# Performance work log

Hardware: AMD Instinct MI355X
Metric: run time of the kernel (lower is better)

Reference implementation:

```python
import jax, jax.numpy as jnp
import numpy as np

B, S, DIN, DOUT = 8, 2048, 512, 512

def setup_inputs() -> dict:
    key = jax.random.key(0)
    ks = jax.random.split(key, 9)
    s = 1.0 / np.sqrt(DIN)  # torch Linear default init scale
    return {
        "Q": jax.random.normal(ks[0], (B, S, DIN), jnp.float32),
        "K": jax.random.normal(ks[1], (B, S, DIN), jnp.float32),
        "V": jax.random.normal(ks[2], (B, S, DIN), jnp.float32),
        "Wq": jax.random.uniform(ks[3], (DIN, DOUT), jnp.float32, -s, s),
        "bq": jax.random.uniform(ks[4], (DOUT,), jnp.float32, -s, s),
        "Wk": jax.random.uniform(ks[5], (DIN, DOUT), jnp.float32, -s, s),
        "bk": jax.random.uniform(ks[6], (DOUT,), jnp.float32, -s, s),
        "Wv": jax.random.uniform(ks[7], (DIN, DOUT), jnp.float32, -s, s),
        "bv": jax.random.uniform(ks[8], (DOUT,), jnp.float32, -s, s),
    }

def reference(Q, K, V, Wq, bq, Wk, bk, Wv, bv):
    q = Q @ Wq + bq  # [B,S,D]
    k = K @ Wk + bk
    v = V @ Wv + bv
    # Unscaled attention, exactly as in the torch module
    attn = jnp.einsum('bqd,bkd->bqk', q, k)  # [B,S,S]
    attn_prob = jax.nn.softmax(attn, axis=-1)
    return jnp.einsum('bqk,bkd->bqd', attn_prob, v)
```

## Files before the change

kernel.cpp:

```cpp
#include <hip/hip_runtime.h>
#include <hip/hip_bf16.h>
#include <hip/hip_fp16.h>

#define B_ 8
#define S_ 2048
#define D_ 512

typedef _Float16 f16x8 __attribute__((ext_vector_type(8)));
typedef float f32x4 __attribute__((ext_vector_type(4)));

__device__ __forceinline__ void gload16(const void* g, void* l) {
    __builtin_amdgcn_global_load_lds(
        (const __attribute__((address_space(1))) void*)g,
        (__attribute__((address_space(3))) void*)l, 16, 0, 0);
}

__global__ void wconv_kernel(const float* __restrict__ Wq,
                             const float* __restrict__ Wk,
                             const float* __restrict__ Wv,
                             _Float16* __restrict__ w_ws) {
    int idx = blockIdx.x * 256 + threadIdx.x;
    int which = blockIdx.y;
    const float* W = (which == 0) ? Wq : (which == 1) ? Wk : Wv;
    int n = idx >> 9;
    int k = idx & 511;
    w_ws[(size_t)which * D_ * D_ + (size_t)n * D_ + k] = (_Float16)W[(size_t)k * D_ + n];
}

__launch_bounds__(256)
__global__ void proj_kernel(const float* __restrict__ Q,
                            const float* __restrict__ K,
                            const float* __restrict__ V,
                            const _Float16* __restrict__ w_ws,
                            const float* __restrict__ bq,
                            const float* __restrict__ bk,
                            const float* __restrict__ bv,
                            _Float16* __restrict__ q_ws,
                            _Float16* __restrict__ k_ws,
                            _Float16* __restrict__ v_ws) {
    __shared__ __align__(16) float    As[128 * 32];
    __shared__ __align__(16) _Float16 Bs[128 * 32];

    const int which = blockIdx.z;
    const float* X    = (which == 0) ? Q  : (which == 1) ? K  : V;
    const float* bias = (which == 0) ? bq : (which == 1) ? bk : bv;
    const _Float16* Wt = w_ws + (size_t)which * D_ * D_;

    const int Nb = blockIdx.x * 128;
    const int Mb = blockIdx.y * 128;
    const int t = threadIdx.x;
    const int w = t >> 6;
    const int l = t & 63;
    const int lr = l & 15;
    const int lk = (l >> 4) * 8;
    const int lq = (l >> 4) * 4;

    f32x4 acc[2][8] = {};

    for (int k0 = 0; k0 < D_; k0 += 32) {
        {
            int c = t;
#pragma unroll
            for (int i = 0; i < 4; i++, c += 256) {
                int row = c >> 3, p = c & 7;
                gload16(X + (size_t)(Mb + row) * D_ + k0 + ((p ^ (row & 7)) << 2),
                        As + c * 4);
            }
        }
        {
            int c = t;
#pragma unroll
            for (int i = 0; i < 2; i++, c += 256) {
                int col = c >> 2, p = c & 3;
                gload16(Wt + (size_t)(Nb + col) * D_ + k0 + ((p ^ (col & 3)) << 3),
                        Bs + c * 8);
            }
        }
        __syncthreads();

        f16x8 a[2], b[8];
#pragma unroll
        for (int mi = 0; mi < 2; mi++) {
            int row = w * 32 + mi * 16 + lr;
            int s0 = lk >> 2;
            const float* base = As + row * 32;
            f32x4 a0 = *(const f32x4*)(base + ((s0 ^ (row & 7)) << 2));
            f32x4 a1 = *(const f32x4*)(base + (((s0 + 1) ^ (row & 7)) << 2));
#pragma unroll
            for (int j = 0; j < 4; j++) { a[mi][j] = (_Float16)a0[j]; a[mi][4 + j] = (_Float16)a1[j]; }
        }
#pragma unroll
        for (int ni = 0; ni < 8; ni++) {
            int col = ni * 16 + lr;
            int s = lk >> 3;
            b[ni] = *(const f16x8*)(Bs + col * 32 + ((s ^ (col & 3)) << 3));
        }
#pragma unroll
        for (int mi = 0; mi < 2; mi++)
#pragma unroll
            for (int ni = 0; ni < 8; ni++)
                acc[mi][ni] = __builtin_amdgcn_mfma_f32_16x16x32_f16(a[mi], b[ni], acc[mi][ni], 0, 0, 0);
        __syncthreads();
    }

#pragma unroll
    for (int ni = 0; ni < 8; ni++) {
        int col = Nb + ni * 16 + lr;
        float bn = bias[col];
#pragma unroll
        for (int mi = 0; mi < 2; mi++) {
#pragma unroll
            for (int j = 0; j < 4; j++) {
                int row = Mb + w * 32 + mi * 16 + lq + j;
                float vv = acc[mi][ni][j] + bn;
                if (which == 0) {
                    q_ws[(size_t)row * D_ + col] = (_Float16)vv;
                } else if (which == 1) {
                    k_ws[(size_t)row * D_ + col] = (_Float16)vv;
                } else {
                    int bb = row >> 11, s = row & 2047;
                    v_ws[((size_t)bb * D_ + col) * S_ + s] = (_Float16)vv;
                }
            }
        }
    }
}

__launch_bounds__(1024)
__global__ void attn_kernel(const _Float16* __restrict__ q_ws,
                            const _Float16* __restrict__ k_ws,
                            const _Float16* __restrict__ v_ws,
                            float* __restrict__ out) {
    __shared__ float    S_lds[64][260];
    __shared__ _Float16 P_lds[64][264];
    __shared__ float    m_lds[64];
    __shared__ float    l_lds[64];
    __shared__ float    alpha_lds[64];

    const int bid = blockIdx.x;
    const int b  = bid & 7;
    const int qb = (bid >> 3) * 64;

    const int t = threadIdx.x;
    const int w = t >> 6;
    const int l = t & 63;
    const int qg = w >> 3;
    const int kc = w & 7;
    const int lr = l & 15;
    const int lk = (l >> 4) * 8;
    const int lq = (l >> 4) * 4;

    const _Float16* qp = q_ws + (size_t)b * S_ * D_;
    const _Float16* kp = k_ws + (size_t)b * S_ * D_;
    const _Float16* vp = v_ws + (size_t)b * D_ * S_;

    if (t < 64) { m_lds[t] = -INFINITY; l_lds[t] = 0.f; }

    f32x4 oacc[2][4] = {};
    __syncthreads();

    for (int kv0 = 0; kv0 < S_; kv0 += 256) {
        f32x4 sacc[2][2] = {};
        for (int d0 = 0; d0 < D_; d0 += 32) {
            f16x8 aq[2], bk2[2];
#pragma unroll
            for (int mi = 0; mi < 2; mi++)
                aq[mi] = *(const f16x8*)(qp + (size_t)(qb + qg * 32 + mi * 16 + lr) * D_ + d0 + lk);
#pragma unroll
            for (int ni = 0; ni < 2; ni++)
                bk2[ni] = *(const f16x8*)(kp + (size_t)(kv0 + kc * 32 + ni * 16 + lr) * D_ + d0 + lk);
#pragma unroll
            for (int mi = 0; mi < 2; mi++)
#pragma unroll
                for (int ni = 0; ni < 2; ni++)
                    sacc[mi][ni] = __builtin_amdgcn_mfma_f32_16x16x32_f16(aq[mi], bk2[ni], sacc[mi][ni], 0, 0, 0);
        }
#pragma unroll
        for (int mi = 0; mi < 2; mi++)
#pragma unroll
            for (int ni = 0; ni < 2; ni++)
#pragma unroll
                for (int j = 0; j < 4; j++)
                    S_lds[qg * 32 + mi * 16 + lq + j][kc * 32 + ni * 16 + lr] = sacc[mi][ni][j];
        __syncthreads();

        {
            const int r = t >> 4;
            const int cs = (t & 15) * 16;
            float sv[16];
#pragma unroll
            for (int c4 = 0; c4 < 4; c4++)
                *(float4*)&sv[c4 * 4] = *(const float4*)&S_lds[r][cs + c4 * 4];
            float mx = sv[0];
#pragma unroll
            for (int c = 1; c < 16; c++) mx = fmaxf(mx, sv[c]);
            mx = fmaxf(mx, __shfl_xor(mx, 1));
            mx = fmaxf(mx, __shfl_xor(mx, 2));
            mx = fmaxf(mx, __shfl_xor(mx, 4));
            mx = fmaxf(mx, __shfl_xor(mx, 8));
            float m_old = m_lds[r];
            float m_new = fmaxf(m_old, mx);
            float ps = 0.f;
            f16x8 p0, p1;
#pragma unroll
            for (int c = 0; c < 8; c++) {
                float p = __expf(sv[c] - m_new);
                ps += p;
                p0[c] = (_Float16)p;
            }
#pragma unroll
            for (int c = 0; c < 8; c++) {
                float p = __expf(sv[c + 8] - m_new);
                ps += p;
                p1[c] = (_Float16)p;
            }
            *(f16x8*)&P_lds[r][cs]     = p0;
            *(f16x8*)&P_lds[r][cs + 8] = p1;
            ps += __shfl_xor(ps, 1);
            ps += __shfl_xor(ps, 2);
            ps += __shfl_xor(ps, 4);
            ps += __shfl_xor(ps, 8);
            if ((t & 15) == 0) {
                float al = __expf(m_old - m_new);
                alpha_lds[r] = al;
                l_lds[r] = l_lds[r] * al + ps;
                m_lds[r] = m_new;
            }
        }
        __syncthreads();

#pragma unroll
        for (int mi = 0; mi < 2; mi++)
#pragma unroll
            for (int j = 0; j < 4; j++) {
                float al = alpha_lds[qg * 32 + mi * 16 + lq + j];
#pragma unroll
                for (int ni = 0; ni < 4; ni++) oacc[mi][ni][j] *= al;
            }

        for (int ks = 0; ks < 8; ks++) {
            f16x8 pa[2], vb[4];
#pragma unroll
            for (int mi = 0; mi < 2; mi++)
                pa[mi] = *(const f16x8*)&P_lds[qg * 32 + mi * 16 + lr][ks * 32 + lk];
#pragma unroll
            for (int ni = 0; ni < 4; ni++)
                vb[ni] = *(const f16x8*)(vp + (size_t)(kc * 64 + ni * 16 + lr) * S_ + kv0 + ks * 32 + lk);
#pragma unroll
            for (int mi = 0; mi < 2; mi++)
#pragma unroll
                for (int ni = 0; ni < 4; ni++)
                    oacc[mi][ni] = __builtin_amdgcn_mfma_f32_16x16x32_f16(pa[mi], vb[ni], oacc[mi][ni], 0, 0, 0);
        }
    }

#pragma unroll
    for (int mi = 0; mi < 2; mi++)
#pragma unroll
        for (int j = 0; j < 4; j++) {
            int row = qg * 32 + mi * 16 + lq + j;
            float rl = 1.f / l_lds[row];
#pragma unroll
            for (int ni = 0; ni < 4; ni++) {
                int col = kc * 64 + ni * 16 + lr;
                out[((size_t)b * S_ + qb + row) * D_ + col] = oacc[mi][ni][j] * rl;
            }
        }
}

extern "C" void kernel_launch(void* const* d_in, const int* in_sizes, int n_in,
                              void* d_out, int out_size, void* d_ws, size_t ws_size,
                              hipStream_t stream) {
    const float* Q  = (const float*)d_in[0];
    const float* K  = (const float*)d_in[1];
    const float* V  = (const float*)d_in[2];
    const float* Wq = (const float*)d_in[3];
    const float* bq = (const float*)d_in[4];
    const float* Wk = (const float*)d_in[5];
    const float* bk = (const float*)d_in[6];
    const float* Wv = (const float*)d_in[7];
    const float* bv = (const float*)d_in[8];
    float* out = (float*)d_out;

    char* ws = (char*)d_ws;
    _Float16* w_ws = (_Float16*)ws;
    _Float16* q_ws = (_Float16*)(ws + 3ull * 512 * 512 * 2);
    _Float16* k_ws = q_ws + 8ull * 2048 * 512;
    _Float16* v_ws = k_ws + 8ull * 2048 * 512;

    wconv_kernel<<<dim3(1024, 3), 256, 0, stream>>>(Wq, Wk, Wv, w_ws);
    proj_kernel<<<dim3(4, 128, 3), 256, 0, stream>>>(Q, K, V, w_ws, bq, bk, bv, q_ws, k_ws, v_ws);
    attn_kernel<<<dim3(256), 1024, 0, stream>>>(q_ws, k_ws, v_ws, out);
}
```

Before: 556.8 us.

## Halve attention query tile, stage Q in LDS, alias P into S buffer

The attention kernel now uses 32-row query tiles with 512 threads per block, which doubles the grid to 512 blocks so more blocks fit on the GPU. Q for the tile is loaded once into LDS via global_load_lds instead of being re-read from global memory for every KV chunk. The P buffer is stored inside the padding and tail of the S rows to cut LDS use, and a barrier is added at the end of each iteration to protect that aliasing. The trade-off is that each K/V element is now loaded by twice as many blocks, raising global/L2 traffic per unit of work.

```diff
diff --git a/kernel.cpp b/kernel.cpp
--- a/kernel.cpp
+++ b/kernel.cpp
@@ -126,26 +126,25 @@
     }
 }
 
-__launch_bounds__(1024)
+__launch_bounds__(512, 4)
 __global__ void attn_kernel(const _Float16* __restrict__ q_ws,
                             const _Float16* __restrict__ k_ws,
                             const _Float16* __restrict__ v_ws,
                             float* __restrict__ out) {
-    __shared__ float    S_lds[64][260];
-    __shared__ _Float16 P_lds[64][264];
-    __shared__ float    m_lds[64];
-    __shared__ float    l_lds[64];
-    __shared__ float    alpha_lds[64];
+    __shared__ __align__(16) float    S_lds[32][260];
+    __shared__ __align__(16) _Float16 Q_lds[16384];
+    __shared__ float m_lds[32];
+    __shared__ float l_lds[32];
+    __shared__ float alpha_lds[32];
 
     const int bid = blockIdx.x;
     const int b  = bid & 7;
-    const int qb = (bid >> 3) * 64;
+    const int qb = (bid >> 3) * 32;
 
     const int t = threadIdx.x;
     const int w = t >> 6;
     const int l = t & 63;
-    const int qg = w >> 3;
-    const int kc = w & 7;
+    const int kc = w;
     const int lr = l & 15;
     const int lk = (l >> 4) * 8;
     const int lq = (l >> 4) * 4;
@@ -154,18 +153,27 @@
     const _Float16* kp = k_ws + (size_t)b * S_ * D_;
     const _Float16* vp = v_ws + (size_t)b * D_ * S_;
 
-    if (t < 64) { m_lds[t] = -INFINITY; l_lds[t] = 0.f; }
+#pragma unroll
+    for (int i = 0; i < 4; i++) {
+        int pi = w * 4 + i;
+        int ds = pi >> 1, mi = pi & 1;
+        gload16(qp + (size_t)(qb + mi * 16 + lr) * D_ + ds * 32 + lk,
+                Q_lds + pi * 512 + l * 8);
+    }
+    if (t < 32) { m_lds[t] = -INFINITY; l_lds[t] = 0.f; }
 
     f32x4 oacc[2][4] = {};
     __syncthreads();
 
     for (int kv0 = 0; kv0 < S_; kv0 += 256) {
         f32x4 sacc[2][2] = {};
+#pragma unroll 4
         for (int d0 = 0; d0 < D_; d0 += 32) {
+            int ds = d0 >> 5;
             f16x8 aq[2], bk2[2];
 #pragma unroll
             for (int mi = 0; mi < 2; mi++)
-                aq[mi] = *(const f16x8*)(qp + (size_t)(qb + qg * 32 + mi * 16 + lr) * D_ + d0 + lk);
+                aq[mi] = *(const f16x8*)(Q_lds + (ds * 2 + mi) * 512 + l * 8);
 #pragma unroll
             for (int ni = 0; ni < 2; ni++)
                 bk2[ni] = *(const f16x8*)(kp + (size_t)(kv0 + kc * 32 + ni * 16 + lr) * D_ + d0 + lk);
@@ -181,7 +189,7 @@
             for (int ni = 0; ni < 2; ni++)
 #pragma unroll
                 for (int j = 0; j < 4; j++)
-                    S_lds[qg * 32 + mi * 16 + lq + j][kc * 32 + ni * 16 + lr] = sacc[mi][ni][j];
+                    S_lds[mi * 16 + lq + j][kc * 32 + ni * 16 + lr] = sacc[mi][ni][j];
         __syncthreads();
 
         {
@@ -214,8 +222,9 @@
                 ps += p;
                 p1[c] = (_Float16)p;
             }
-            *(f16x8*)&P_lds[r][cs]     = p0;
-            *(f16x8*)&P_lds[r][cs + 8] = p1;
+            char* prow = (char*)&S_lds[r][0] + 528;
+            *(f16x8*)(prow + cs * 2)      = p0;
+            *(f16x8*)(prow + cs * 2 + 16) = p1;
             ps += __shfl_xor(ps, 1);
             ps += __shfl_xor(ps, 2);
             ps += __shfl_xor(ps, 4);
@@ -233,16 +242,17 @@
         for (int mi = 0; mi < 2; mi++)
 #pragma unroll
             for (int j = 0; j < 4; j++) {
-                float al = alpha_lds[qg * 32 + mi * 16 + lq + j];
+                float al = alpha_lds[mi * 16 + lq + j];
 #pragma unroll
                 for (int ni = 0; ni < 4; ni++) oacc[mi][ni][j] *= al;
             }
 
+#pragma unroll 2
         for (int ks = 0; ks < 8; ks++) {
             f16x8 pa[2], vb[4];
 #pragma unroll
             for (int mi = 0; mi < 2; mi++)
-                pa[mi] = *(const f16x8*)&P_lds[qg * 32 + mi * 16 + lr][ks * 32 + lk];
+                pa[mi] = *(const f16x8*)((const char*)&S_lds[mi * 16 + lr][0] + 528 + (ks * 32 + lk) * 2);
 #pragma unroll
             for (int ni = 0; ni < 4; ni++)
                 vb[ni] = *(const f16x8*)(vp + (size_t)(kc * 64 + ni * 16 + lr) * S_ + kv0 + ks * 32 + lk);
@@ -252,13 +262,14 @@
                 for (int ni = 0; ni < 4; ni++)
                     oacc[mi][ni] = __builtin_amdgcn_mfma_f32_16x16x32_f16(pa[mi], vb[ni], oacc[mi][ni], 0, 0, 0);
         }
+        __syncthreads();
     }
 
 #pragma unroll
     for (int mi = 0; mi < 2; mi++)
 #pragma unroll
         for (int j = 0; j < 4; j++) {
-            int row = qg * 32 + mi * 16 + lq + j;
+            int row = mi * 16 + lq + j;
             float rl = 1.f / l_lds[row];
 #pragma unroll
             for (int ni = 0; ni < 4; ni++) {
@@ -290,5 +301,5 @@
 
     wconv_kernel<<<dim3(1024, 3), 256, 0, stream>>>(Wq, Wk, Wv, w_ws);
     proj_kernel<<<dim3(4, 128, 3), 256, 0, stream>>>(Q, K, V, w_ws, bq, bk, bv, q_ws, k_ws, v_ws);
-    attn_kernel<<<dim3(256), 1024, 0, stream>>>(q_ws, k_ws, v_ws, out);
-}
+    attn_kernel<<<dim3(512), 512, 0, stream>>>(q_ws, k_ws, v_ws, out);
+}
```

Result: faster. 449.4 us (-19.3%).
